# Kernel optimization log

Hardware: AMD Instinct MI355X
Metric: run time of the kernel (lower is better)

Reference implementation:

```python
import jax, jax.numpy as jnp
import numpy as np

H = 8       # n_heads
E = 128     # embedding_size (= per-head dim)
NEG = -1000000000.0


def setup_inputs() -> dict:
    key = jax.random.key(0)
    ks = jax.random.split(key, 12)
    b, n = 8, 1024
    x = jax.random.normal(ks[0], (b, n, E), dtype=jnp.float32)
    dist = jax.random.normal(ks[1], (b, n, n), dtype=jnp.float32)
    mask = jax.random.randint(ks[2], (b, n), 0, 2).astype(jnp.float32)
    s = 1.0 / np.sqrt(E)
    Wq = jax.random.normal(ks[3], (E, H * E), dtype=jnp.float32) * s
    Wk = jax.random.normal(ks[4], (E, H * E), dtype=jnp.float32) * s
    Wv = jax.random.normal(ks[5], (E, H * E), dtype=jnp.float32) * s
    bq = jnp.zeros((H * E,), jnp.float32)
    bk = jnp.zeros((H * E,), jnp.float32)
    bv = jnp.zeros((H * E,), jnp.float32)
    Wo = jax.random.normal(ks[6], (H * E, E), dtype=jnp.float32) * (1.0 / np.sqrt(H * E))
    bo = jnp.zeros((E,), jnp.float32)
    return {"x": x, "dist": dist, "mask": mask, "Wq": Wq, "bq": bq,
            "Wk": Wk, "bk": bk, "Wv": Wv, "bv": bv, "Wo": Wo, "bo": bo}


def reference(x, dist, mask, Wq, bq, Wk, bk, Wv, bv, Wo, bo):
    b, n, e = x.shape
    scale = e ** (-0.5)
    # project and split heads: [b, n, H*E] -> [b, H, n, E]
    def heads(W, bias):
        return (x @ W + bias).reshape(b, n, H, e).transpose(0, 2, 1, 3)
    q = heads(Wq, bq) * mask[:, None, :, None]
    k = heads(Wk, bk) * mask[:, None, :, None]
    v = heads(Wv, bv) * mask[:, None, :, None]
    # scores with additive distance bias broadcast over heads
    a = jnp.einsum('bhqe,bhke->bhqk', q * scale, k) + dist[:, None, :, :]
    am = jnp.einsum('bq,bk->bqk', mask, mask)[:, None, :, :]  # [b,1,n,n]
    a = jnp.where(am == 0, NEG, a)
    a = jax.nn.softmax(a, axis=-1)
    a = jnp.where(am == 0, 0.0, a)
    y = jnp.einsum('bhqk,bhke->bhqe', a, v)
    y = y.transpose(0, 2, 1, 3).reshape(b, n, H * e)
    y = y @ Wo + bo
    return y * mask[:, :, None]
```

## Files before the change

### kernel.cpp

```cpp
#include <hip/hip_runtime.h>
#include <hip/hip_bf16.h>
#include <hip/hip_fp16.h>

#define NH 8
#define ED 128
#define NB 8
#define NN 1024

typedef __attribute__((ext_vector_type(8))) short s16x8;
typedef __attribute__((ext_vector_type(8))) __bf16 bf16x8_t;
typedef __attribute__((ext_vector_type(4))) float f32x4;
typedef __attribute__((ext_vector_type(16))) float f32x16;
typedef __attribute__((ext_vector_type(4))) unsigned int u32x4;

static __device__ __forceinline__ unsigned short f2bf(float f) {
    union { float f; unsigned u; } v; v.f = f;
    unsigned r = v.u + 0x7fffu + ((v.u >> 16) & 1u);
    return (unsigned short)(r >> 16);
}

static __device__ __forceinline__ f32x4 mfma16(s16x8 a, s16x8 b, f32x4 c) {
    return __builtin_amdgcn_mfma_f32_16x16x32_bf16(
        __builtin_bit_cast(bf16x8_t, a), __builtin_bit_cast(bf16x8_t, b), c, 0, 0, 0);
}

static __device__ __forceinline__ f32x16 mfma32(s16x8 a, s16x8 b, f32x16 c) {
    return __builtin_amdgcn_mfma_f32_32x32x16_bf16(
        __builtin_bit_cast(bf16x8_t, a), __builtin_bit_cast(bf16x8_t, b), c, 0, 0, 0);
}

static __device__ __forceinline__ unsigned cvtpk(float lo, float hi) {
    unsigned r;
    asm("v_cvt_pk_bf16_f32 %0, %1, %2" : "=v"(r) : "v"(lo), "v"(hi));
    return r;
}

static __device__ __forceinline__ void gll16(const void* g, void* l) {
    __builtin_amdgcn_global_load_lds((const __attribute__((address_space(1))) void*)g,
                                     (__attribute__((address_space(3))) void*)l, 16, 0, 0);
}

__global__ __launch_bounds__(256) void prep_kernel(
    const float* __restrict__ x,
    const float* __restrict__ Wq, const float* __restrict__ Wk,
    const float* __restrict__ Wv, const float* __restrict__ Wo,
    unsigned short* __restrict__ xb,
    unsigned short* __restrict__ wqt, unsigned short* __restrict__ wkt,
    unsigned short* __restrict__ wvt, unsigned short* __restrict__ wot) {
    int bid = blockIdx.x, tid = threadIdx.x;
    if (bid < 1024) {
        int i = bid * 256 + tid;
        float4 v = ((const float4*)x)[i];
        unsigned long long pk = (unsigned long long)f2bf(v.x)
                              | ((unsigned long long)f2bf(v.y) << 16)
                              | ((unsigned long long)f2bf(v.z) << 32)
                              | ((unsigned long long)f2bf(v.w) << 48);
        ((unsigned long long*)xb)[i] = pk;
        return;
    }
    const float* in; unsigned short* outp; int rows_in, cols_in, i;
    if (bid < 1536)      { in = Wq; outp = wqt; rows_in = 128;  cols_in = 1024; i = (bid - 1024) * 256 + tid; }
    else if (bid < 2048) { in = Wk; outp = wkt; rows_in = 128;  cols_in = 1024; i = (bid - 1536) * 256 + tid; }
    else if (bid < 2560) { in = Wv; outp = wvt; rows_in = 128;  cols_in = 1024; i = (bid - 2048) * 256 + tid; }
    else                 { in = Wo; outp = wot; rows_in = 1024; cols_in = 128;  i = (bid - 2560) * 256 + tid; }
    int c = i / rows_in;
    int r = i - c * rows_in;
    outp[i] = f2bf(in[(size_t)r * cols_in + c]);
}

__global__ __launch_bounds__(256) void prep_dist_kernel(
    const float* __restrict__ dist,
    const float* __restrict__ mask,
    unsigned short* __restrict__ dswz) {
    int bid = blockIdx.x;
    int c = bid & 3;
    int t = bid >> 2;
    int kt = t & 15; t >>= 4;
    int qt = t & 7;
    int b = t >> 3;
    int tid = threadIdx.x;
    int h = (tid >> 5) & 1;
    int row = qt * 128 + (tid >> 6) * 32 + (tid & 31);
    int colbase = kt * 64 + (c >> 1) * 32 + (c & 1) * 16 + 4 * h;

    const float* dr = dist + ((size_t)b * NN + row) * NN;
    const float* mr = mask + (size_t)b * NN;
    f32x4 dA = *(const f32x4*)(dr + colbase);
    f32x4 dB = *(const f32x4*)(dr + colbase + 8);
    f32x4 mA = *(const f32x4*)(mr + colbase);
    f32x4 mB = *(const f32x4*)(mr + colbase + 8);

    unsigned short o[8];
#pragma unroll
    for (int jj = 0; jj < 4; ++jj) {
        o[jj]     = (mA[jj] == 0.0f) ? (unsigned short)0xFBFF
                                     : __half_as_ushort(__float2half_rn(dA[jj]));
        o[4 + jj] = (mB[jj] == 0.0f) ? (unsigned short)0xFBFF
                                     : __half_as_ushort(__float2half_rn(dB[jj]));
    }
    u32x4 pk;
    pk[0] = (unsigned)o[0] | ((unsigned)o[1] << 16);
    pk[1] = (unsigned)o[2] | ((unsigned)o[3] << 16);
    pk[2] = (unsigned)o[4] | ((unsigned)o[5] << 16);
    pk[3] = (unsigned)o[6] | ((unsigned)o[7] << 16);
    *(u32x4*)(dswz + ((size_t)bid * 256 + tid) * 8) = pk;
}

__global__ __launch_bounds__(256) void qkv_kernel(
    const unsigned short* __restrict__ xb,
    const unsigned short* __restrict__ wqt,
    const unsigned short* __restrict__ wkt,
    const unsigned short* __restrict__ wvt,
    const float* __restrict__ bq, const float* __restrict__ bk, const float* __restrict__ bv,
    unsigned short* __restrict__ q_ws,
    unsigned short* __restrict__ k_ws,
    unsigned short* __restrict__ v_ws) {
    int bid = blockIdx.x;
    int mt = bid / 24, c = bid % 24;
    int which = c >> 3;
    int c0 = (c & 7) * 128;
    int m0 = mt * 128;
    int tid = threadIdx.x;
    int w = tid >> 6, lane = tid & 63, g = lane >> 4, r15 = lane & 15;
    int wr = (w >> 1) * 64, wc = (w & 1) * 64;

    const unsigned short* wt = (which == 0) ? wqt : (which == 1) ? wkt : wvt;
    const float* bias = (which == 0) ? bq : (which == 1) ? bk : bv;

    const f32x4 fzero = {0.f, 0.f, 0.f, 0.f};
    f32x4 acc[4][4];
#pragma unroll
    for (int i = 0; i < 4; i++)
#pragma unroll
        for (int j = 0; j < 4; j++) acc[i][j] = fzero;

#pragma unroll
    for (int kf = 0; kf < 4; kf++) {
        s16x8 af[4], bfr[4];
#pragma unroll
        for (int mf = 0; mf < 4; mf++)
            af[mf] = *(const s16x8*)(xb + (size_t)(m0 + wr + mf * 16 + r15) * ED + kf * 32 + g * 8);
#pragma unroll
        for (int nf = 0; nf < 4; nf++)
            bfr[nf] = *(const s16x8*)(wt + (size_t)(c0 + wc + nf * 16 + r15) * ED + kf * 32 + g * 8);
#pragma unroll
        for (int mf = 0; mf < 4; mf++)
#pragma unroll
            for (int nf = 0; nf < 4; nf++)
                acc[mf][nf] = mfma16(af[mf], bfr[nf], acc[mf][nf]);
    }

    float scale = (which == 0) ? 0.08838834764831845f : 1.0f;

#pragma unroll
    for (int nf = 0; nf < 4; nf++) {
        int col = c0 + wc + nf * 16 + r15;
        float bv_ = bias[col];
        int hh = col >> 7, e = col & 127;
#pragma unroll
        for (int mf = 0; mf < 4; mf++) {
#pragma unroll
            for (int rr = 0; rr < 4; rr++) {
                int row = m0 + wr + mf * 16 + g * 4 + rr;
                int bb = row >> 10, n = row & 1023;
                int bh = bb * NH + hh;
                float val = (acc[mf][nf][rr] + bv_) * scale;
                if (which == 0) {
                    q_ws[((size_t)bh * NN + n) * ED + e] = f2bf(val);
                } else if (which == 1) {
                    int ktl = n >> 6, k = n & 63;
                    int slot = (e >> 4) * 128 + ((e >> 3) & 1) * 64 + (k >> 5) * 32 + (k & 31);
                    k_ws[(size_t)(bh * 16 + ktl) * 8192 + slot * 8 + (e & 7)] = f2bf(val);
                } else {
                    int ktl = n >> 6, k = n & 63;
                    int slot = (k >> 4) * 256 + ((k >> 3) & 1) * 128 + (e >> 5) * 32 + (e & 31);
                    v_ws[(size_t)(bh * 16 + ktl) * 8192 + slot * 8 + (k & 7)] = f2bf(val);
                }
            }
        }
    }
}

__global__ __launch_bounds__(256) void attn_kernel(
    const unsigned short* __restrict__ q_ws,
    const unsigned short* __restrict__ k_ws,
    const unsigned short* __restrict__ v_ws,
    const unsigned short* __restrict__ dswz,
    unsigned short* __restrict__ y_ws) {
    int p = blockIdx.x;
    int b = p & 7, r = p >> 3;
    int head = r >> 3, qt = r & 7;
    int bh = b * NH + head;
    int q0 = qt * 128;

    int tid = threadIdx.x;
    int w = tid >> 6, lane = tid & 63;
    int e31 = lane & 31, h = lane >> 5;
    bool h0 = (h == 0);

    __shared__ __align__(16) unsigned short Kl[2][8192];
    __shared__ __align__(16) unsigned short Vl[2][8192];

    const char* kg = (const char*)k_ws + (size_t)bh * 16 * 16384;
    const char* vg = (const char*)v_ws + (size_t)bh * 16 * 16384;
    const char* dq = (const char*)dswz + ((size_t)(b * 8 + qt) << 18);

    int qrow = q0 + w * 32 + e31;
    s16x8 qf[8];
    const unsigned short* qb = q_ws + ((size_t)bh * NN + qrow) * ED + h * 8;
#pragma unroll
    for (int es = 0; es < 8; ++es) qf[es] = *(const s16x8*)(qb + es * 16);

    const f32x16 fz16 = {0.f,0.f,0.f,0.f,0.f,0.f,0.f,0.f,0.f,0.f,0.f,0.f,0.f,0.f,0.f,0.f};
    f32x16 o0 = fz16, o1 = fz16, o2 = fz16, o3 = fz16;
    float l_r = 0.f;

#pragma unroll
    for (int pass = 0; pass < 4; ++pass) {
        gll16(kg + (pass * 256 + tid) * 16, (char*)&Kl[0][0] + pass * 4096 + w * 1024);
        gll16(vg + (pass * 256 + tid) * 16, (char*)&Vl[0][0] + pass * 4096 + w * 1024);
    }
    __syncthreads();

    for (int kt = 0; kt < 16; ++kt) {
        int cur = kt & 1;
        if (kt < 15) {
            const char* kn = kg + (size_t)(kt + 1) * 16384;
            const char* vn = vg + (size_t)(kt + 1) * 16384;
            char* kd = (char*)&Kl[cur ^ 1][0] + w * 1024;
            char* vd = (char*)&Vl[cur ^ 1][0] + w * 1024;
#pragma unroll
            for (int pass = 0; pass < 4; ++pass) {
                gll16(kn + (pass * 256 + tid) * 16, kd + pass * 4096);
                gll16(vn + (pass * 256 + tid) * 16, vd + pass * 4096);
            }
        }

        u32x4 dch[4];
#pragma unroll
        for (int c = 0; c < 4; ++c)
            dch[c] = *(const u32x4*)(dq + ((size_t)(kt * 4 + c) * 256 + tid) * 16);

        const char* Kp = (const char*)&Kl[cur][0] + h * 1024 + e31 * 16;
        f32x16 sA0 = fz16, sA1 = fz16;
#pragma unroll
        for (int es = 0; es < 8; ++es) {
            s16x8 kb0 = *(const s16x8*)(Kp + es * 2048);
            s16x8 kb1 = *(const s16x8*)(Kp + es * 2048 + 512);
            sA0 = mfma32(kb0, qf[es], sA0);
            sA1 = mfma32(kb1, qf[es], sA1);
        }

        float pp[32];
#pragma unroll
        for (int c = 0; c < 4; ++c) {
#pragma unroll
            for (int u = 0; u < 8; ++u) {
                int i = c * 8 + u;
                unsigned wv = dch[c][u >> 1];
                float dv = __half2float(__ushort_as_half(
                    (unsigned short)((u & 1) ? (wv >> 16) : (wv & 0xffff))));
                float sv = (i < 16) ? sA0[i] : sA1[i - 16];
                float pv = __expf(sv + dv - 16.0f);
                pp[i] = pv;
                l_r += pv;
            }
        }

        const char* Vp = (const char*)&Vl[cur][0] + h * 2048 + e31 * 16;
#pragma unroll
        for (int kf = 0; kf < 2; ++kf) {
#pragma unroll
            for (int ks2 = 0; ks2 < 2; ++ks2) {
                const float* pb = &pp[kf * 16 + ks2 * 8];
                unsigned X0 = cvtpk(pb[0], pb[1]);
                unsigned X1 = cvtpk(pb[2], pb[3]);
                unsigned Y0 = cvtpk(pb[4], pb[5]);
                unsigned Y1 = cvtpk(pb[6], pb[7]);
                unsigned sx0 = (unsigned)__shfl_xor((int)X0, 32, 64);
                unsigned sx1 = (unsigned)__shfl_xor((int)X1, 32, 64);
                unsigned sy0 = (unsigned)__shfl_xor((int)Y0, 32, 64);
                unsigned sy1 = (unsigned)__shfl_xor((int)Y1, 32, 64);
                u32x4 pw;
                pw[0] = h0 ? X0 : sy0;
                pw[1] = h0 ? X1 : sy1;
                pw[2] = h0 ? sx0 : Y0;
                pw[3] = h0 ? sx1 : Y1;
                s16x8 pa = __builtin_bit_cast(s16x8, pw);
                int kstep = kf * 2 + ks2;
                const char* vp = Vp + kstep * 4096;
                o0 = mfma32(pa, *(const s16x8*)(vp), o0);
                o1 = mfma32(pa, *(const s16x8*)(vp + 512), o1);
                o2 = mfma32(pa, *(const s16x8*)(vp + 1024), o2);
                o3 = mfma32(pa, *(const s16x8*)(vp + 1536), o3);
            }
        }
        __syncthreads();
    }

    float lt = l_r + __shfl_xor(l_r, 32, 64);
    float inv = (lt > 0.f) ? 1.0f / lt : 0.f;
#pragma unroll
    for (int rc = 0; rc < 4; ++rc) {
#pragma unroll
        for (int jj = 0; jj < 4; ++jj) {
            int qq = jj + 8 * rc + 4 * h;
            float iq = __shfl(inv, qq, 64);
            int row = q0 + w * 32 + qq;
            size_t base = ((size_t)b * NN + row) * (NH * ED) + head * ED + e31;
            y_ws[base]      = f2bf(o0[rc * 4 + jj] * iq);
            y_ws[base + 32] = f2bf(o1[rc * 4 + jj] * iq);
            y_ws[base + 64] = f2bf(o2[rc * 4 + jj] * iq);
            y_ws[base + 96] = f2bf(o3[rc * 4 + jj] * iq);
        }
    }
}

__global__ __launch_bounds__(256) void oproj_kernel(
    const unsigned short* __restrict__ y_ws,
    const unsigned short* __restrict__ wot,
    const float* __restrict__ bo,
    const float* __restrict__ mask,
    float* __restrict__ outp) {
    int bid = blockIdx.x;
    int mt = bid >> 1, nt = bid & 1;
    int m0 = mt * 64, c0 = nt * 64;
    int tid = threadIdx.x;
    int w = tid >> 6, lane = tid & 63, g = lane >> 4, r15 = lane & 15;

    const f32x4 fzero = {0.f, 0.f, 0.f, 0.f};
    f32x4 acc[4];
#pragma unroll
    for (int i = 0; i < 4; i++) acc[i] = fzero;

    const unsigned short* arow = y_ws + (size_t)(m0 + w * 16 + r15) * (NH * ED);
    for (int kt = 0; kt < 32; ++kt) {
        s16x8 af = *(const s16x8*)(arow + kt * 32 + g * 8);
#pragma unroll
        for (int nf = 0; nf < 4; nf++) {
            s16x8 bfr = *(const s16x8*)(wot + (size_t)(c0 + nf * 16 + r15) * (NH * ED) + kt * 32 + g * 8);
            acc[nf] = mfma16(af, bfr, acc[nf]);
        }
    }
#pragma unroll
    for (int nf = 0; nf < 4; nf++) {
        int col = c0 + nf * 16 + r15;
        float bias = bo[col];
#pragma unroll
        for (int rr = 0; rr < 4; rr++) {
            int token = m0 + w * 16 + g * 4 + rr;
            outp[(size_t)token * ED + col] = (acc[nf][rr] + bias) * mask[token];
        }
    }
}

extern "C" void kernel_launch(void* const* d_in, const int* in_sizes, int n_in,
                              void* d_out, int out_size, void* d_ws, size_t ws_size,
                              hipStream_t stream) {
    const float* x    = (const float*)d_in[0];
    const float* dist = (const float*)d_in[1];
    const float* mask = (const float*)d_in[2];
    const float* Wq   = (const float*)d_in[3];
    const float* bq   = (const float*)d_in[4];
    const float* Wk   = (const float*)d_in[5];
    const float* bk   = (const float*)d_in[6];
    const float* Wv   = (const float*)d_in[7];
    const float* bv   = (const float*)d_in[8];
    const float* Wo   = (const float*)d_in[9];
    const float* bo   = (const float*)d_in[10];
    float* outp = (float*)d_out;

    char* ws = (char*)d_ws;
    unsigned short* xb   = (unsigned short*)(ws);
    unsigned short* wqt  = (unsigned short*)(ws + (2u << 20));
    unsigned short* wkt  = (unsigned short*)(ws + (2u << 20) + (256u << 10));
    unsigned short* wvt  = (unsigned short*)(ws + (2u << 20) + (512u << 10));
    unsigned short* wot  = (unsigned short*)(ws + (2u << 20) + (768u << 10));
    unsigned short* q_ws = (unsigned short*)(ws + (3u << 20));
    unsigned short* k_ws = (unsigned short*)(ws + (19u << 20));
    unsigned short* v_ws = (unsigned short*)(ws + (35u << 20));
    unsigned short* y_ws = (unsigned short*)(ws + (51u << 20));
    unsigned short* dswz = (unsigned short*)(ws + (67u << 20));

    prep_kernel<<<3072, 256, 0, stream>>>(x, Wq, Wk, Wv, Wo, xb, wqt, wkt, wvt, wot);
    prep_dist_kernel<<<4096, 256, 0, stream>>>(dist, mask, dswz);
    qkv_kernel<<<1536, 256, 0, stream>>>(xb, wqt, wkt, wvt, bq, bk, bv, q_ws, k_ws, v_ws);
    attn_kernel<<<512, 256, 0, stream>>>(q_ws, k_ws, v_ws, dswz, y_ws);
    oproj_kernel<<<256, 256, 0, stream>>>(y_ws, wot, bo, mask, outp);
}
```

Before: 136.0 us.

## Stage dist tiles through LDS, prefetch next dist chunk, fold log2e into exp2

prep_dist_kernel now has each block load a 128x64 dist tile into shared memory with coalesced float4 reads, then emit four swizzled fp16 chunks, so it launches a quarter as many blocks. The attention kernel double-buffers the dist chunk in registers, loading the next tile's values during the current iteration through a two-step unrolled lambda. The softmax is rewritten to use exp2 directly: log2e is folded into the q scale and the dist values, and the -16 offset is moved into the MFMA accumulator initial value. Together these aim to cut uncoalesced global traffic and hide dist load latency, at the cost of more registers and an extra LDS pass in the prep step.

```diff
diff --git a/kernel.cpp b/kernel.cpp
--- a/kernel.cpp
+++ b/kernel.cpp
@@ -12,6 +12,9 @@
 typedef __attribute__((ext_vector_type(4))) float f32x4;
 typedef __attribute__((ext_vector_type(16))) float f32x16;
 typedef __attribute__((ext_vector_type(4))) unsigned int u32x4;
+
+#define LOG2E 1.4426950408889634f
+#define SINIT -23.083120654223414f
 
 static __device__ __forceinline__ unsigned short f2bf(float f) {
     union { float f; unsigned u; } v; v.f = f;
@@ -73,37 +76,48 @@
     const float* __restrict__ mask,
     unsigned short* __restrict__ dswz) {
     int bid = blockIdx.x;
-    int c = bid & 3;
-    int t = bid >> 2;
-    int kt = t & 15; t >>= 4;
+    int kt = bid & 15;
+    int t = bid >> 4;
     int qt = t & 7;
     int b = t >> 3;
     int tid = threadIdx.x;
+
+    __shared__ float dtile[128][65];
+    __shared__ float mrow[64];
+
+    {
+        int seg = tid & 15;
+        int r0 = tid >> 4;
+        const float* src = dist + ((size_t)b * NN + qt * 128) * NN + kt * 64;
+#pragma unroll
+        for (int pass = 0; pass < 8; ++pass) {
+            int row = pass * 16 + r0;
+            f32x4 v = *(const f32x4*)(src + (size_t)row * NN + seg * 4);
+            *(f32x4*)&dtile[row][seg * 4] = v;
+        }
+        if (tid < 64) mrow[tid] = mask[b * NN + kt * 64 + tid];
+    }
+    __syncthreads();
+
     int h = (tid >> 5) & 1;
-    int row = qt * 128 + (tid >> 6) * 32 + (tid & 31);
-    int colbase = kt * 64 + (c >> 1) * 32 + (c & 1) * 16 + 4 * h;
-
-    const float* dr = dist + ((size_t)b * NN + row) * NN;
-    const float* mr = mask + (size_t)b * NN;
-    f32x4 dA = *(const f32x4*)(dr + colbase);
-    f32x4 dB = *(const f32x4*)(dr + colbase + 8);
-    f32x4 mA = *(const f32x4*)(mr + colbase);
-    f32x4 mB = *(const f32x4*)(mr + colbase + 8);
-
-    unsigned short o[8];
-#pragma unroll
-    for (int jj = 0; jj < 4; ++jj) {
-        o[jj]     = (mA[jj] == 0.0f) ? (unsigned short)0xFBFF
-                                     : __half_as_ushort(__float2half_rn(dA[jj]));
-        o[4 + jj] = (mB[jj] == 0.0f) ? (unsigned short)0xFBFF
-                                     : __half_as_ushort(__float2half_rn(dB[jj]));
-    }
-    u32x4 pk;
-    pk[0] = (unsigned)o[0] | ((unsigned)o[1] << 16);
-    pk[1] = (unsigned)o[2] | ((unsigned)o[3] << 16);
-    pk[2] = (unsigned)o[4] | ((unsigned)o[5] << 16);
-    pk[3] = (unsigned)o[6] | ((unsigned)o[7] << 16);
-    *(u32x4*)(dswz + ((size_t)bid * 256 + tid) * 8) = pk;
+    int row = (tid >> 6) * 32 + (tid & 31);
+#pragma unroll
+    for (int c = 0; c < 4; ++c) {
+        unsigned short o[8];
+#pragma unroll
+        for (int u = 0; u < 8; ++u) {
+            int col = (c >> 1) * 32 + (c & 1) * 16 + 4 * h + (u >> 2) * 8 + (u & 3);
+            float dv = dtile[row][col] * LOG2E;
+            o[u] = (mrow[col] == 0.0f) ? (unsigned short)0xFBFF
+                                       : __half_as_ushort(__float2half_rn(dv));
+        }
+        u32x4 pk;
+        pk[0] = (unsigned)o[0] | ((unsigned)o[1] << 16);
+        pk[1] = (unsigned)o[2] | ((unsigned)o[3] << 16);
+        pk[2] = (unsigned)o[4] | ((unsigned)o[5] << 16);
+        pk[3] = (unsigned)o[6] | ((unsigned)o[7] << 16);
+        *(u32x4*)(dswz + ((size_t)(bid * 4 + c) * 256 + tid) * 8) = pk;
+    }
 }
 
 __global__ __launch_bounds__(256) void qkv_kernel(
@@ -150,7 +164,7 @@
                 acc[mf][nf] = mfma16(af[mf], bfr[nf], acc[mf][nf]);
     }
 
-    float scale = (which == 0) ? 0.08838834764831845f : 1.0f;
+    float scale = (which == 0) ? 0.12751741566380696f : 1.0f;
 
 #pragma unroll
     for (int nf = 0; nf < 4; nf++) {
@@ -212,18 +226,25 @@
     for (int es = 0; es < 8; ++es) qf[es] = *(const s16x8*)(qb + es * 16);
 
     const f32x16 fz16 = {0.f,0.f,0.f,0.f,0.f,0.f,0.f,0.f,0.f,0.f,0.f,0.f,0.f,0.f,0.f,0.f};
+    f32x16 sini;
+#pragma unroll
+    for (int i = 0; i < 16; ++i) sini[i] = SINIT;
     f32x16 o0 = fz16, o1 = fz16, o2 = fz16, o3 = fz16;
     float l_r = 0.f;
+
+    u32x4 dchA[4], dchB[4];
 
 #pragma unroll
     for (int pass = 0; pass < 4; ++pass) {
         gll16(kg + (pass * 256 + tid) * 16, (char*)&Kl[0][0] + pass * 4096 + w * 1024);
         gll16(vg + (pass * 256 + tid) * 16, (char*)&Vl[0][0] + pass * 4096 + w * 1024);
     }
+#pragma unroll
+    for (int c = 0; c < 4; ++c)
+        dchA[c] = *(const u32x4*)(dq + ((size_t)c * 256 + tid) * 16);
     __syncthreads();
 
-    for (int kt = 0; kt < 16; ++kt) {
-        int cur = kt & 1;
+    auto iter = [&](int kt, int cur, u32x4* dU, u32x4* dL) __attribute__((always_inline)) {
         if (kt < 15) {
             const char* kn = kg + (size_t)(kt + 1) * 16384;
             const char* vn = vg + (size_t)(kt + 1) * 16384;
@@ -234,15 +255,13 @@
                 gll16(kn + (pass * 256 + tid) * 16, kd + pass * 4096);
                 gll16(vn + (pass * 256 + tid) * 16, vd + pass * 4096);
             }
-        }
-
-        u32x4 dch[4];
-#pragma unroll
-        for (int c = 0; c < 4; ++c)
-            dch[c] = *(const u32x4*)(dq + ((size_t)(kt * 4 + c) * 256 + tid) * 16);
+#pragma unroll
+            for (int c = 0; c < 4; ++c)
+                dL[c] = *(const u32x4*)(dq + ((size_t)((kt + 1) * 4 + c) * 256 + tid) * 16);
+        }
 
         const char* Kp = (const char*)&Kl[cur][0] + h * 1024 + e31 * 16;
-        f32x16 sA0 = fz16, sA1 = fz16;
+        f32x16 sA0 = sini, sA1 = sini;
 #pragma unroll
         for (int es = 0; es < 8; ++es) {
             s16x8 kb0 = *(const s16x8*)(Kp + es * 2048);
@@ -257,11 +276,11 @@
 #pragma unroll
             for (int u = 0; u < 8; ++u) {
                 int i = c * 8 + u;
-                unsigned wv = dch[c][u >> 1];
+                unsigned wv = dU[c][u >> 1];
                 float dv = __half2float(__ushort_as_half(
                     (unsigned short)((u & 1) ? (wv >> 16) : (wv & 0xffff))));
                 float sv = (i < 16) ? sA0[i] : sA1[i - 16];
-                float pv = __expf(sv + dv - 16.0f);
+                float pv = __builtin_exp2f(sv + dv);
                 pp[i] = pv;
                 l_r += pv;
             }
@@ -296,6 +315,12 @@
             }
         }
         __syncthreads();
+    };
+
+#pragma unroll 1
+    for (int k2 = 0; k2 < 8; ++k2) {
+        iter(2 * k2,     0, dchA, dchB);
+        iter(2 * k2 + 1, 1, dchB, dchA);
     }
 
     float lt = l_r + __shfl_xor(l_r, 32, 64);
@@ -383,7 +408,7 @@
     unsigned short* dswz = (unsigned short*)(ws + (67u << 20));
 
     prep_kernel<<<3072, 256, 0, stream>>>(x, Wq, Wk, Wv, Wo, xb, wqt, wkt, wvt, wot);
-    prep_dist_kernel<<<4096, 256, 0, stream>>>(dist, mask, dswz);
+    prep_dist_kernel<<<1024, 256, 0, stream>>>(dist, mask, dswz);
     qkv_kernel<<<1536, 256, 0, stream>>>(xb, wqt, wkt, wvt, bq, bk, bv, q_ws, k_ws, v_ws);
     attn_kernel<<<512, 256, 0, stream>>>(q_ws, k_ws, v_ws, dswz, y_ws);
     oproj_kernel<<<256, 256, 0, stream>>>(y_ws, wot, bo, mask, outp);
```

Result: slower. 144.0 us (+5.9%).
